# Kernel optimization log

Measured on AMD Instinct MI355X. Metric: run time of the kernel, lower is better.

Reference implementation:

```python
import jax, jax.numpy as jnp
import numpy as np

D_MODEL = 1024
NUM_HEADS = 16
D_K = D_MODEL // NUM_HEADS
D_FF = 4096
LN_EPS = 1e-5


def layer_norm(x, gamma, beta):
    mu = jnp.mean(x, axis=-1, keepdims=True)
    var = jnp.var(x, axis=-1, keepdims=True)
    return (x - mu) * jax.lax.rsqrt(var + LN_EPS) * gamma + beta


def setup_inputs() -> dict:
    key = jax.random.key(0)
    ks = jax.random.split(key, 10)
    s = 0.02
    return {
        "x": jax.random.normal(ks[0], (2, 2048, D_MODEL), dtype=jnp.float32),
        # per-head projections stacked: [H, d_model, d_k] (equivalent to the
        # num_heads separate nn.Linear(d_model, d_k, bias=False) modules)
        "Wq": jax.random.normal(ks[1], (NUM_HEADS, D_MODEL, D_K), dtype=jnp.float32) * s,
        "Wk": jax.random.normal(ks[2], (NUM_HEADS, D_MODEL, D_K), dtype=jnp.float32) * s,
        "Wv": jax.random.normal(ks[3], (NUM_HEADS, D_MODEL, D_K), dtype=jnp.float32) * s,
        "Wo": jax.random.normal(ks[4], (D_MODEL, D_MODEL), dtype=jnp.float32) * s,
        "W1": jax.random.normal(ks[5], (D_MODEL, D_FF), dtype=jnp.float32) * s,
        "b1": jnp.zeros((D_FF,), dtype=jnp.float32),
        "W2": jax.random.normal(ks[6], (D_FF, D_MODEL), dtype=jnp.float32) * s,
        "b2": jnp.zeros((D_MODEL,), dtype=jnp.float32),
        "g1": jnp.ones((D_MODEL,), dtype=jnp.float32),
        "beta1": jnp.zeros((D_MODEL,), dtype=jnp.float32),
        "g2": jnp.ones((D_MODEL,), dtype=jnp.float32),
        "beta2": jnp.zeros((D_MODEL,), dtype=jnp.float32),
    }


def reference(x, Wq, Wk, Wv, Wo, W1, b1, W2, b2, g1, beta1, g2, beta2):
    B, S, D = x.shape
    # ---- pre-LN multi-head self-attention ----
    h = layer_norm(x, g1, beta1)
    # batched QKV projections (equivalent to the per-head Python loop)
    Q = jnp.einsum('bsd,hdk->bhsk', h, Wq)  # [B,H,S,dk]
    K = jnp.einsum('bsd,hdk->bhsk', h, Wk)
    V = jnp.einsum('bsd,hdk->bhsk', h, Wv)
    scores = jnp.einsum('bhqk,bhsk->bhqs', Q, K) / jnp.sqrt(jnp.asarray(D_K, x.dtype))
    weights = jax.nn.softmax(scores, axis=-1)  # [B,H,S,S]
    attn = jnp.einsum('bhqs,bhsk->bhqk', weights, V)  # [B,H,S,dk]
    # concat heads along feature dim (head order preserved)
    concat = attn.transpose(0, 2, 1, 3).reshape(B, S, D)
    x = x + concat @ Wo
    # ---- pre-LN FFN (exact erf GELU, matching nn.GELU default) ----
    h2 = layer_norm(x, g2, beta2)
    ffn = jax.nn.gelu(h2 @ W1 + b1, approximate=False) @ W2 + b2
    return x + ffn
```

## Files before the change

### kernel.cpp

```cpp
#include <hip/hip_runtime.h>
#include <stdint.h>


typedef __attribute__((ext_vector_type(8))) short bf16x8;
typedef __attribute__((ext_vector_type(4))) float f32x4;
typedef __attribute__((ext_vector_type(16))) float f32x16;
typedef __attribute__((ext_vector_type(4))) unsigned short u16x4;
typedef __attribute__((ext_vector_type(4))) unsigned int u32x4;

#define DEV __device__ __forceinline__

static constexpr int DM   = 1024;
static constexpr int DFF  = 4096;
static constexpr int NH   = 16;
static constexpr int DKH  = 64;
static constexpr int SEQ  = 2048;
static constexpr int NBAT = 2;
static constexpr int NTOK = NBAT * SEQ;

DEV unsigned short f2bf(float f) {
  union { float f; unsigned int u; } v; v.f = f;
  unsigned int u = v.u;
  return (unsigned short)((u + 0x7fffu + ((u >> 16) & 1u)) >> 16);
}

DEV void gload_lds16(const unsigned short* g, unsigned short* l) {
  __builtin_amdgcn_global_load_lds(
      (const __attribute__((address_space(1))) unsigned int*)g,
      (__attribute__((address_space(3))) unsigned int*)l, 16, 0, 0);
}

DEV float fast_gelu(float x) {
  const float z = fabsf(x) * 0.70710678118654752f;
  const float t = __builtin_amdgcn_rcpf(1.0f + 0.3275911f * z);
  float p = 1.061405429f;
  p = p * t - 1.453152027f;
  p = p * t + 1.421413741f;
  p = p * t - 0.284496736f;
  p = p * t + 0.254829592f;
  p = p * t;
  float erfv = 1.0f - p * __expf(-z * z);
  erfv = copysignf(erfv, x);
  return 0.5f * x * (1.0f + erfv);
}

__global__ __launch_bounds__(256) void ln_kernel(
    const float* __restrict__ x, const float* __restrict__ g,
    const float* __restrict__ be, unsigned short* __restrict__ out) {
  const int row = blockIdx.x;
  const int t = threadIdx.x;
  const int lane = t & 63, w = t >> 6;
  const float4* xr = (const float4*)(x + (size_t)row * DM);
  float4 v = xr[t];
  float s  = v.x + v.y + v.z + v.w;
  float s2 = v.x * v.x + v.y * v.y + v.z * v.z + v.w * v.w;
#pragma unroll
  for (int off = 32; off; off >>= 1) {
    s  += __shfl_down(s, off);
    s2 += __shfl_down(s2, off);
  }
  __shared__ float rs_[4], rq_[4];
  if (lane == 0) { rs_[w] = s; rq_[w] = s2; }
  __syncthreads();
  float fs = rs_[0] + rs_[1] + rs_[2] + rs_[3];
  float fq = rq_[0] + rq_[1] + rq_[2] + rq_[3];
  float mu = fs * (1.0f / DM);
  float var = fq * (1.0f / DM) - mu * mu;
  float rstd = rsqrtf(var + 1e-5f);
  float4 gv = ((const float4*)g)[t];
  float4 bv = ((const float4*)be)[t];
  u16x4 o;
  o[0] = f2bf((v.x - mu) * rstd * gv.x + bv.x);
  o[1] = f2bf((v.y - mu) * rstd * gv.y + bv.y);
  o[2] = f2bf((v.z - mu) * rstd * gv.z + bv.z);
  o[3] = f2bf((v.w - mu) * rstd * gv.w + bv.w);
  *(u16x4*)(out + (size_t)row * DM + t * 4) = o;
}

__global__ __launch_bounds__(256) void transpose_weights(
    const float* __restrict__ Wq, const float* __restrict__ Wk,
    const float* __restrict__ Wv, const float* __restrict__ Wo,
    const float* __restrict__ W1, const float* __restrict__ W2,
    unsigned short* __restrict__ wqkv_t, unsigned short* __restrict__ wo_t,
    unsigned short* __restrict__ w1_t, unsigned short* __restrict__ w2_t) {
  __shared__ float lds[64][65];
  const int t = blockIdx.x;
  const float* inb; unsigned short* outb; int in_ld, out_ld;
  if (t < 768) {
    const int slice = t >> 4, tin = t & 15;
    const int which = slice >> 4, h = slice & 15;
    const float* W = (which == 0) ? Wq : (which == 1) ? Wk : Wv;
    inb = W + (size_t)((h << 10) + (tin << 6)) * 64;
    in_ld = 64;
    outb = wqkv_t + ((size_t)((which << 10) + (h << 6)) << 10) + (tin << 6);
    out_ld = 1024;
  } else if (t < 1024) {
    const int tt = t - 768, tr = tt >> 4, tc = tt & 15;
    inb = Wo + (size_t)(tc << 6) * 1024 + (tr << 6); in_ld = 1024;
    outb = wo_t + (size_t)(tr << 6) * 1024 + (tc << 6); out_ld = 1024;
  } else if (t < 2048) {
    const int tt = t - 1024, tr = tt >> 4, tc = tt & 15;
    inb = W1 + (size_t)(tc << 6) * 4096 + (tr << 6); in_ld = 4096;
    outb = w1_t + (size_t)(tr << 6) * 1024 + (tc << 6); out_ld = 1024;
  } else {
    const int tt = t - 2048, tr = tt >> 6, tc = tt & 63;
    inb = W2 + (size_t)(tc << 6) * 1024 + (tr << 6); in_ld = 1024;
    outb = w2_t + (size_t)(tr << 6) * 4096 + (tc << 6); out_ld = 4096;
  }
  const int j = threadIdx.x & 63, i0 = threadIdx.x >> 6;
#pragma unroll
  for (int p = 0; p < 16; ++p) {
    const int i = i0 + p * 4;
    lds[j][i] = inb[(size_t)i * in_ld + j];
  }
  __syncthreads();
#pragma unroll
  for (int p = 0; p < 16; ++p) {
    const int r = i0 + p * 4;
    outb[(size_t)r * out_ld + j] = f2bf(lds[r][j]);
  }
}

struct EpiArgs {
  unsigned short* q;
  unsigned short* k;
  unsigned short* vt;
  unsigned short* ob16;
  float* of32;
  float* p0;
  const float* bias;
  const float* resid;
};

template <int EPI>
DEV void epilogue_elem(float v, int row, int col, int N, int bz,
                       const EpiArgs& ep) {
  if constexpr (EPI == 0) {
    const int bb = row >> 11, rr = row & 2047;
    if (col < 1024) {
      const int hh = col >> 6, dk = col & 63;
      const int kk = dk >> 4, h8 = (dk >> 3) & 1, e = dk & 7;
      const int qblk = rr >> 5, l31 = rr & 31;
      ep.q[((size_t)(bb * NH + hh) * 64 + qblk) * 2048 + kk * 512 +
           (h8 * 32 + l31) * 8 + e] = f2bf(v * 0.18033688011112042f);
    } else if (col < 2048) {
      const int c = col - 1024;
      const int hh = c >> 6, dk = c & 63;
      const int kk = dk >> 4, h8 = (dk >> 3) & 1, e = dk & 7;
      const int kvblk = rr >> 5, l31 = rr & 31;
      ep.k[((size_t)(bb * NH + hh) * 64 + kvblk) * 2048 + kk * 512 +
           (h8 * 32 + l31) * 8 + e] = f2bf(v);
    } else {
      const int c = col - 2048, hh = c >> 6, dd = c & 63;
      const int ssw = (rr & ~12) | ((rr & 4) << 1) | ((rr & 8) >> 1);
      const int t64 = ssw >> 6, w = (ssw >> 4) & 3;
      const int h8 = (ssw >> 3) & 1, e = ssw & 7;
      const int dblk = dd >> 5, l31 = dd & 31;
      ep.vt[(((size_t)(bb * NH + hh) * 32 + t64) * 8 + dblk * 4 + w) * 512 +
            (h8 * 32 + l31) * 8 + e] = f2bf(v);
    }
  } else if constexpr (EPI == 1) {
    const size_t idx = (size_t)row * N + col;
    ep.of32[idx] = v + ep.resid[idx];
  } else if constexpr (EPI == 2) {
    ep.ob16[(size_t)row * N + col] = f2bf(fast_gelu(v + ep.bias[col]));
  } else {
    const size_t idx = (size_t)row * N + col;
    if (bz == 0) ep.p0[idx] = v;
    else ep.of32[idx] = ep.of32[idx] + v + ep.bias[col];
  }
}

template <int EPI>
__global__ __launch_bounds__(512, 2) void gemm_256(
    const unsigned short* __restrict__ A, const unsigned short* __restrict__ Bt,
    int N, int K, int ldk, EpiArgs ep) {
  __shared__ __align__(16) unsigned short Als[2][256 * 64];
  __shared__ __align__(16) unsigned short Bls[2][256 * 64];
  const int t = threadIdx.x, lane = t & 63, wave = t >> 6;
  const int wm = wave >> 2, wn = wave & 3;
  const int g = lane >> 4, r16 = lane & 15;
  const int nx = gridDim.x, nwg = nx * gridDim.y;
  int wgid = blockIdx.y * nx + blockIdx.x;
  wgid = (wgid & 7) * (nwg >> 3) + (wgid >> 3);
  const int m0 = (wgid / nx) * 256, n0 = (wgid % nx) * 256;

  f32x4 acc[8][4];
  const f32x4 z4 = {0.f, 0.f, 0.f, 0.f};
#pragma unroll
  for (int i = 0; i < 8; ++i)
#pragma unroll
    for (int j = 0; j < 4; ++j) acc[i][j] = z4;

  auto stage_half = [&](int b, int k0, int h) {
#pragma unroll
    for (int i = 0; i < 2; ++i) {
      const int c = i * 512 + t;
      const int row = c >> 3;
      const int sc = ((c & 7) ^ (row & 7)) * 8;
      const int dofs = ((h & 1) << 13) + (i * 512 + (wave << 6)) * 8;
      if (h < 2)
        gload_lds16(A + (size_t)(m0 + ((h & 1) << 7) + row) * ldk + k0 + sc,
                    &Als[b][dofs]);
      else
        gload_lds16(Bt + (size_t)(n0 + ((h & 1) << 7) + row) * ldk + k0 + sc,
                    &Bls[b][dofs]);
    }
  };

  const int NT = K >> 6;
#pragma unroll
  for (int h = 0; h < 4; ++h) stage_half(0, 0, h);

  for (int kt = 0; kt < NT; ++kt) {
    const int cur = kt & 1;
    const bool more = (kt + 1) < NT;
    const int nk0 = (kt + 1) << 6;
    __builtin_amdgcn_s_barrier();
    if (more) {
      stage_half(cur ^ 1, nk0, 0);
      stage_half(cur ^ 1, nk0, 1);
      asm volatile("s_waitcnt vmcnt(4)" ::: "memory");
    } else {
      asm volatile("s_waitcnt vmcnt(0)" ::: "memory");
    }
    __builtin_amdgcn_s_barrier();
    __builtin_amdgcn_sched_barrier(0);

    bf16x8 Af[8][2];
#pragma unroll
    for (int mf = 0; mf < 8; ++mf) {
      const int row = (wm << 7) + (mf << 4) + r16;
#pragma unroll
      for (int ks = 0; ks < 2; ++ks)
        Af[mf][ks] = *(const bf16x8*)
            &Als[cur][row * 64 + ((((ks << 2) | g) ^ (row & 7)) << 3)];
    }
#pragma unroll
    for (int qn = 0; qn < 2; ++qn) {
      bf16x8 Bf[2][2];
#pragma unroll
      for (int ni = 0; ni < 2; ++ni) {
        const int row = (wn << 6) + (((qn << 1) | ni) << 4) + r16;
#pragma unroll
        for (int ks = 0; ks < 2; ++ks)
          Bf[ni][ks] = *(const bf16x8*)
              &Bls[cur][row * 64 + ((((ks << 2) | g) ^ (row & 7)) << 3)];
      }
      __builtin_amdgcn_s_setprio(1);
#pragma unroll
      for (int ks = 0; ks < 2; ++ks)
#pragma unroll
        for (int mf = 0; mf < 8; ++mf)
#pragma unroll
          for (int ni = 0; ni < 2; ++ni)
            acc[mf][(qn << 1) | ni] = __builtin_amdgcn_mfma_f32_16x16x32_bf16(
                Af[mf][ks], Bf[ni][ks], acc[mf][(qn << 1) | ni], 0, 0, 0);
      __builtin_amdgcn_s_setprio(0);
      if (qn == 0 && more) {
        stage_half(cur ^ 1, nk0, 2);
        stage_half(cur ^ 1, nk0, 3);
      }
    }
  }
#pragma unroll
  for (int mf = 0; mf < 8; ++mf)
#pragma unroll
    for (int nf = 0; nf < 4; ++nf)
#pragma unroll
      for (int r = 0; r < 4; ++r)
        epilogue_elem<EPI>(acc[mf][nf][r],
                           m0 + (wm << 7) + (mf << 4) + (g << 2) + r,
                           n0 + (wn << 6) + (nf << 4) + r16, N, 0, ep);
}

template <int EPI>
__global__ __launch_bounds__(256) void gemm_pipe(
    const unsigned short* __restrict__ A, const unsigned short* __restrict__ Bt,
    int N, int Kc, int ldk, EpiArgs ep) {
  __shared__ __align__(16) unsigned short Als[2][128 * 64];
  __shared__ __align__(16) unsigned short Bls[2][128 * 64];
  const int t = threadIdx.x, lane = t & 63, wave = t >> 6;
  const int wm = wave >> 1, wn = wave & 1;
  const int g = lane >> 4, r16 = lane & 15;
  const int nx = gridDim.x;
  const int nwg = nx * gridDim.y;
  int wgid = blockIdx.y * nx + blockIdx.x;
  wgid = (wgid & 7) * (nwg >> 3) + (wgid >> 3);
  const int m0 = (wgid / nx) * 128, n0 = (wgid % nx) * 128;
  const int kbase = blockIdx.z * Kc;

  f32x4 acc[4][4];
  const f32x4 z4 = {0.f, 0.f, 0.f, 0.f};
#pragma unroll
  for (int i = 0; i < 4; ++i)
#pragma unroll
    for (int j = 0; j < 4; ++j) acc[i][j] = z4;

  auto stage = [&](int b, int k0) {
#pragma unroll
    for (int i = 0; i < 4; ++i) {
      const int cb = i * 256 + wave * 64;
      const int c = cb + lane;
      const int row = c >> 3;
      const int sc = ((c & 7) ^ (row & 7)) * 8;
      gload_lds16(A + (size_t)(m0 + row) * ldk + kbase + k0 + sc, &Als[b][cb * 8]);
      gload_lds16(Bt + (size_t)(n0 + row) * ldk + kbase + k0 + sc, &Bls[b][cb * 8]);
    }
  };

  const int NT = Kc >> 6;
  stage(0, 0);
  __syncthreads();
  for (int kt = 0; kt < NT; ++kt) {
    const int cur = kt & 1;
    if (kt + 1 < NT) stage(cur ^ 1, (kt + 1) << 6);
    const int sw = r16 & 7;
    bf16x8 af[2][4], bfr[2][4];
#pragma unroll
    for (int ks = 0; ks < 2; ++ks) {
#pragma unroll
      for (int mt = 0; mt < 4; ++mt)
        af[ks][mt] = *(const bf16x8*)&Als[cur][(wm * 64 + mt * 16 + r16) * 64 +
                                              (((ks << 2) | g) ^ sw) * 8];
#pragma unroll
      for (int nt = 0; nt < 4; ++nt)
        bfr[ks][nt] = *(const bf16x8*)&Bls[cur][(wn * 64 + nt * 16 + r16) * 64 +
                                               (((ks << 2) | g) ^ sw) * 8];
    }
    __builtin_amdgcn_s_setprio(1);
#pragma unroll
    for (int ks = 0; ks < 2; ++ks)
#pragma unroll
      for (int mt = 0; mt < 4; ++mt)
#pragma unroll
        for (int nt = 0; nt < 4; ++nt)
          acc[mt][nt] = __builtin_amdgcn_mfma_f32_16x16x32_bf16(
              af[ks][mt], bfr[ks][nt], acc[mt][nt], 0, 0, 0);
    __builtin_amdgcn_s_setprio(0);
    __syncthreads();
  }
#pragma unroll
  for (int mt = 0; mt < 4; ++mt)
#pragma unroll
    for (int nt = 0; nt < 4; ++nt)
#pragma unroll
      for (int r = 0; r < 4; ++r)
        epilogue_elem<EPI>(acc[mt][nt][r], m0 + wm * 64 + mt * 16 + g * 4 + r,
                           n0 + wn * 64 + nt * 16 + r16, N, blockIdx.z, ep);
}

__global__ __launch_bounds__(256) void reduce_add(const float* __restrict__ p,
                                                  float* __restrict__ out) {
  const int i = blockIdx.x * 256 + threadIdx.x;
  float4 a = ((const float4*)p)[i];
  float4 b = ((float4*)out)[i];
  b.x += a.x; b.y += a.y; b.z += a.z; b.w += a.w;
  ((float4*)out)[i] = b;
}

struct AttnState {
  f32x16 o0, o1;
  float m, lsum;
};

DEV void load_k(const unsigned short* kbase, int s, bf16x8 k0[4], bf16x8 k1[4]) {
  const unsigned short* p = kbase + (size_t)(s >> 5) * 2048;
#pragma unroll
  for (int kk = 0; kk < 4; ++kk) {
    k0[kk] = *(const bf16x8*)(p + kk * 512);
    k1[kk] = *(const bf16x8*)(p + 2048 + kk * 512);
  }
}

DEV void attn_tile(const bf16x8 k0[4], const bf16x8 k1[4],
                   const bf16x8 v0[4], const bf16x8 v1[4],
                   const bf16x8 qf[4], AttnState& st) {
  const f32x16 z16 = {0.f};
  f32x16 pA = z16, pB = z16;
  __builtin_amdgcn_s_setprio(1);
#pragma unroll
  for (int kk = 0; kk < 4; ++kk) {
    pA = __builtin_amdgcn_mfma_f32_32x32x16_bf16(k0[kk], qf[kk], pA, 0, 0, 0);
    pB = __builtin_amdgcn_mfma_f32_32x32x16_bf16(k1[kk], qf[kk], pB, 0, 0, 0);
  }
  __builtin_amdgcn_s_setprio(0);
  float m0 = fmaxf(pA[0], pB[0]), m1 = fmaxf(pA[1], pB[1]);
  float m2 = fmaxf(pA[2], pB[2]), m3 = fmaxf(pA[3], pB[3]);
#pragma unroll
  for (int r = 4; r < 16; r += 4) {
    m0 = fmaxf(m0, fmaxf(pA[r + 0], pB[r + 0]));
    m1 = fmaxf(m1, fmaxf(pA[r + 1], pB[r + 1]));
    m2 = fmaxf(m2, fmaxf(pA[r + 2], pB[r + 2]));
    m3 = fmaxf(m3, fmaxf(pA[r + 3], pB[r + 3]));
  }
  float mx = fmaxf(fmaxf(m0, m1), fmaxf(m2, m3));
  mx = fmaxf(mx, __shfl_xor(mx, 32));
  if (__any(mx > st.m + 11.5416f)) {
    const float mnew = fmaxf(st.m, mx);
    const float corr = exp2f(st.m - mnew);
#pragma unroll
    for (int r = 0; r < 16; ++r) { st.o0[r] *= corr; st.o1[r] *= corr; }
    st.lsum *= corr;
    st.m = mnew;
  }
  float ps = 0.f;
#pragma unroll
  for (int r = 0; r < 16; ++r) {
    pA[r] = exp2f(pA[r] - st.m); ps += pA[r];
    pB[r] = exp2f(pB[r] - st.m); ps += pB[r];
  }
  ps += __shfl_xor(ps, 32);
  st.lsum += ps;
  bf16x8 pw[4];
#pragma unroll
  for (int w = 0; w < 4; ++w) {
    unsigned int wd0, wd1, wd2, wd3;
    const int e0 = (w & 1) * 8;
    if (w < 2) {
      asm("v_cvt_pk_bf16_f32 %0, %1, %2" : "=v"(wd0) : "v"(pA[e0 + 0]), "v"(pA[e0 + 1]));
      asm("v_cvt_pk_bf16_f32 %0, %1, %2" : "=v"(wd1) : "v"(pA[e0 + 2]), "v"(pA[e0 + 3]));
      asm("v_cvt_pk_bf16_f32 %0, %1, %2" : "=v"(wd2) : "v"(pA[e0 + 4]), "v"(pA[e0 + 5]));
      asm("v_cvt_pk_bf16_f32 %0, %1, %2" : "=v"(wd3) : "v"(pA[e0 + 6]), "v"(pA[e0 + 7]));
    } else {
      asm("v_cvt_pk_bf16_f32 %0, %1, %2" : "=v"(wd0) : "v"(pB[e0 + 0]), "v"(pB[e0 + 1]));
      asm("v_cvt_pk_bf16_f32 %0, %1, %2" : "=v"(wd1) : "v"(pB[e0 + 2]), "v"(pB[e0 + 3]));
      asm("v_cvt_pk_bf16_f32 %0, %1, %2" : "=v"(wd2) : "v"(pB[e0 + 4]), "v"(pB[e0 + 5]));
      asm("v_cvt_pk_bf16_f32 %0, %1, %2" : "=v"(wd3) : "v"(pB[e0 + 6]), "v"(pB[e0 + 7]));
    }
    u32x4 wv = {wd0, wd1, wd2, wd3};
    pw[w] = __builtin_bit_cast(bf16x8, wv);
  }
  __builtin_amdgcn_s_setprio(1);
#pragma unroll
  for (int w = 0; w < 4; ++w) {
    st.o0 = __builtin_amdgcn_mfma_f32_32x32x16_bf16(v0[w], pw[w], st.o0, 0, 0, 0);
    st.o1 = __builtin_amdgcn_mfma_f32_32x32x16_bf16(v1[w], pw[w], st.o1, 0, 0, 0);
  }
  __builtin_amdgcn_s_setprio(0);
}

__global__ __launch_bounds__(256, 2) void attn_kernel(
    const unsigned short* __restrict__ Qc, const unsigned short* __restrict__ Kc,
    const unsigned short* __restrict__ Vt, unsigned short* __restrict__ Oc) {
  const int lane = threadIdx.x & 63, wave = threadIdx.x >> 6;
  const int hi = lane >> 5, l31 = lane & 31;
  const int i = blockIdx.x;
  const int k8 = i & 7, mq = i >> 3;
  const int grp = k8 + 8 * (mq >> 4);
  const int qb = mq & 15;
  const int b = grp >> 4, h = grp & 15;
  const int q0 = qb * 128 + wave * 32;

  const unsigned short* qbp = Qc + ((size_t)grp * 64 + (q0 >> 5)) * 2048 + lane * 8;
  const unsigned short* kbp = Kc + (size_t)grp * 64 * 2048 + lane * 8;
  const unsigned short* vbp = Vt + (size_t)grp * 32 * 4096 + lane * 8;

  bf16x8 qf[4];
#pragma unroll
  for (int kk = 0; kk < 4; ++kk) qf[kk] = *(const bf16x8*)(qbp + kk * 512);

  AttnState st;
#pragma unroll
  for (int r = 0; r < 16; ++r) { st.o0[r] = 0.f; st.o1[r] = 0.f; }
  st.m = -1e30f; st.lsum = 0.f;

  bf16x8 kA0[4], kA1[4], kB0[4], kB1[4];
  load_k(kbp, 0, kA0, kA1);

  for (int s0 = 0; s0 < SEQ; s0 += 128) {
    const unsigned short* vt0 = vbp + (size_t)(s0 >> 6) * 4096;
    bf16x8 v0[4], v1[4];
#pragma unroll
    for (int w = 0; w < 4; ++w) {
      v0[w] = *(const bf16x8*)(vt0 + w * 512);
      v1[w] = *(const bf16x8*)(vt0 + 2048 + w * 512);
    }
    load_k(kbp, s0 + 64, kB0, kB1);
    attn_tile(kA0, kA1, v0, v1, qf, st);
    const unsigned short* vt1 = vbp + (size_t)((s0 + 64) >> 6) * 4096;
#pragma unroll
    for (int w = 0; w < 4; ++w) {
      v0[w] = *(const bf16x8*)(vt1 + w * 512);
      v1[w] = *(const bf16x8*)(vt1 + 2048 + w * 512);
    }
    const int snext = (s0 + 128 < SEQ) ? (s0 + 128) : 0;
    load_k(kbp, snext, kA0, kA1);
    attn_tile(kB0, kB1, v0, v1, qf, st);
  }

  const float inv = 1.0f / st.lsum;
  const size_t rowbase = (size_t)b * SEQ;
  unsigned short* op = Oc + (rowbase + q0 + l31) * DM + h * DKH + hi * 4;
#pragma unroll
  for (int dblk = 0; dblk < 2; ++dblk)
#pragma unroll
    for (int g4 = 0; g4 < 4; ++g4) {
      u16x4 stv;
#pragma unroll
      for (int r = 0; r < 4; ++r) {
        const float v = (dblk ? st.o1[g4 * 4 + r] : st.o0[g4 * 4 + r]) * inv;
        stv[r] = f2bf(v);
      }
      *(u16x4*)(op + dblk * 32 + g4 * 8) = stv;
    }
}

extern "C" void kernel_launch(void* const* d_in, const int* in_sizes, int n_in,
                              void* d_out, int out_size, void* d_ws,
                              size_t ws_size, hipStream_t stream) {
  (void)in_sizes; (void)n_in; (void)out_size; (void)ws_size;
  const float* x   = (const float*)d_in[0];
  const float* Wq  = (const float*)d_in[1];
  const float* Wk  = (const float*)d_in[2];
  const float* Wv  = (const float*)d_in[3];
  const float* Wo  = (const float*)d_in[4];
  const float* W1  = (const float*)d_in[5];
  const float* b1  = (const float*)d_in[6];
  const float* W2  = (const float*)d_in[7];
  const float* b2  = (const float*)d_in[8];
  const float* g1  = (const float*)d_in[9];
  const float* be1 = (const float*)d_in[10];
  const float* g2  = (const float*)d_in[11];
  const float* be2 = (const float*)d_in[12];
  float* out = (float*)d_out;

  char* ws = (char*)d_ws;
  const size_t MB = 1024 * 1024;
  unsigned short* h_buf  = (unsigned short*)(ws + 0 * MB);
  unsigned short* wqkv_t = (unsigned short*)(ws + 8 * MB);
  unsigned short* wo_t   = (unsigned short*)(ws + 14 * MB);
  unsigned short* w1_t   = (unsigned short*)(ws + 16 * MB);
  unsigned short* w2_t   = (unsigned short*)(ws + 24 * MB);
  unsigned short* q_attn = (unsigned short*)(ws + 32 * MB);
  unsigned short* k_attn = (unsigned short*)(ws + 40 * MB);
  unsigned short* v_attn = (unsigned short*)(ws + 48 * MB);
  unsigned short* ffn1   = (unsigned short*)(ws + 32 * MB);
  float*          p0     = (float*)(ws + 0 * MB);

  EpiArgs e0 = {}; e0.q = q_attn; e0.k = k_attn; e0.vt = v_attn;
  EpiArgs e1 = {}; e1.of32 = out; e1.resid = x;
  EpiArgs e2 = {}; e2.ob16 = ffn1; e2.bias = b1;
  EpiArgs e4 = {}; e4.of32 = out; e4.p0 = p0; e4.bias = b2;

  transpose_weights<<<3072, 256, 0, stream>>>(Wq, Wk, Wv, Wo, W1, W2,
                                              wqkv_t, wo_t, w1_t, w2_t);
  ln_kernel<<<NTOK, 256, 0, stream>>>(x, g1, be1, h_buf);
  gemm_256<0><<<dim3(3072 / 256, NTOK / 256), 512, 0, stream>>>(
      h_buf, wqkv_t, 3072, DM, DM, e0);
  attn_kernel<<<512, 256, 0, stream>>>(q_attn, k_attn, v_attn, h_buf);
  gemm_pipe<1><<<dim3(DM / 128, NTOK / 128, 1), 256, 0, stream>>>(
      h_buf, wo_t, DM, DM, DM, e1);
  ln_kernel<<<NTOK, 256, 0, stream>>>(out, g2, be2, h_buf);
  gemm_256<2><<<dim3(DFF / 256, NTOK / 256), 512, 0, stream>>>(
      h_buf, w1_t, DFF, DM, DM, e2);
  gemm_pipe<4><<<dim3(DM / 128, NTOK / 128, 2), 256, 0, stream>>>(
      ffn1, w2_t, DM, DFF / 2, DFF, e4);
  reduce_add<<<4096, 256, 0, stream>>>(p0, out);
}
```

Before: 264.7 us.

## Split attention KV range across two wave halves and merge softmax states in LDS

The attention kernel now launches 512 threads per block. The two halves of the waves each process half of the key/value sequence for the same query rows, and their partial max, sum and output accumulators are merged through shared memory before the store. This doubles the waves available per CU for the 512-block grid, which is meant to hide latency in the attention phase. It adds an LDS round-trip, a block barrier and a merge step. The exp2f calls are also replaced with the hardware exp2 builtin.

```diff
diff --git a/kernel.cpp b/kernel.cpp
--- a/kernel.cpp
+++ b/kernel.cpp
@@ -398,7 +398,7 @@
   mx = fmaxf(mx, __shfl_xor(mx, 32));
   if (__any(mx > st.m + 11.5416f)) {
     const float mnew = fmaxf(st.m, mx);
-    const float corr = exp2f(st.m - mnew);
+    const float corr = __builtin_amdgcn_exp2f(st.m - mnew);
 #pragma unroll
     for (int r = 0; r < 16; ++r) { st.o0[r] *= corr; st.o1[r] *= corr; }
     st.lsum *= corr;
@@ -407,8 +407,8 @@
   float ps = 0.f;
 #pragma unroll
   for (int r = 0; r < 16; ++r) {
-    pA[r] = exp2f(pA[r] - st.m); ps += pA[r];
-    pB[r] = exp2f(pB[r] - st.m); ps += pB[r];
+    pA[r] = __builtin_amdgcn_exp2f(pA[r] - st.m); ps += pA[r];
+    pB[r] = __builtin_amdgcn_exp2f(pB[r] - st.m); ps += pB[r];
   }
   ps += __shfl_xor(ps, 32);
   st.lsum += ps;
@@ -440,17 +440,19 @@
   __builtin_amdgcn_s_setprio(0);
 }
 
-__global__ __launch_bounds__(256, 2) void attn_kernel(
+__global__ __launch_bounds__(512, 4) void attn_kernel(
     const unsigned short* __restrict__ Qc, const unsigned short* __restrict__ Kc,
     const unsigned short* __restrict__ Vt, unsigned short* __restrict__ Oc) {
-  const int lane = threadIdx.x & 63, wave = threadIdx.x >> 6;
+  const int t = threadIdx.x;
+  const int lane = t & 63, wave = t >> 6;
+  const int qw = wave & 3, half = wave >> 2;
   const int hi = lane >> 5, l31 = lane & 31;
   const int i = blockIdx.x;
   const int k8 = i & 7, mq = i >> 3;
   const int grp = k8 + 8 * (mq >> 4);
   const int qb = mq & 15;
   const int b = grp >> 4, h = grp & 15;
-  const int q0 = qb * 128 + wave * 32;
+  const int q0 = qb * 128 + qw * 32;
 
   const unsigned short* qbp = Qc + ((size_t)grp * 64 + (q0 >> 5)) * 2048 + lane * 8;
   const unsigned short* kbp = Kc + (size_t)grp * 64 * 2048 + lane * 8;
@@ -465,10 +467,11 @@
   for (int r = 0; r < 16; ++r) { st.o0[r] = 0.f; st.o1[r] = 0.f; }
   st.m = -1e30f; st.lsum = 0.f;
 
+  const int sbase = half << 10;
   bf16x8 kA0[4], kA1[4], kB0[4], kB1[4];
-  load_k(kbp, 0, kA0, kA1);
-
-  for (int s0 = 0; s0 < SEQ; s0 += 128) {
+  load_k(kbp, sbase, kA0, kA1);
+
+  for (int s0 = sbase; s0 < sbase + 1024; s0 += 128) {
     const unsigned short* vt0 = vbp + (size_t)(s0 >> 6) * 4096;
     bf16x8 v0[4], v1[4];
 #pragma unroll
@@ -484,26 +487,46 @@
       v0[w] = *(const bf16x8*)(vt1 + w * 512);
       v1[w] = *(const bf16x8*)(vt1 + 2048 + w * 512);
     }
-    const int snext = (s0 + 128 < SEQ) ? (s0 + 128) : 0;
+    const int snext = (s0 + 128 < sbase + 1024) ? (s0 + 128) : sbase;
     load_k(kbp, snext, kA0, kA1);
     attn_tile(kB0, kB1, v0, v1, qf, st);
   }
 
-  const float inv = 1.0f / st.lsum;
-  const size_t rowbase = (size_t)b * SEQ;
-  unsigned short* op = Oc + (rowbase + q0 + l31) * DM + h * DKH + hi * 4;
-#pragma unroll
-  for (int dblk = 0; dblk < 2; ++dblk)
-#pragma unroll
-    for (int g4 = 0; g4 < 4; ++g4) {
-      u16x4 stv;
-#pragma unroll
-      for (int r = 0; r < 4; ++r) {
-        const float v = (dblk ? st.o1[g4 * 4 + r] : st.o0[g4 * 4 + r]) * inv;
-        stv[r] = f2bf(v);
+  __shared__ float mls[4][2][64];
+  __shared__ float obuf[4][64][33];
+  if (half == 1) {
+    mls[qw][0][lane] = st.m;
+    mls[qw][1][lane] = st.lsum;
+#pragma unroll
+    for (int r = 0; r < 16; ++r) {
+      obuf[qw][lane][r] = st.o0[r];
+      obuf[qw][lane][16 + r] = st.o1[r];
+    }
+  }
+  __syncthreads();
+  if (half == 0) {
+    const float mb = mls[qw][0][lane], lb = mls[qw][1][lane];
+    const float mm = fmaxf(st.m, mb);
+    const float ca = __builtin_amdgcn_exp2f(st.m - mm);
+    const float cb = __builtin_amdgcn_exp2f(mb - mm);
+    const float inv = 1.0f / (st.lsum * ca + lb * cb);
+    const size_t rowbase = (size_t)b * SEQ;
+    unsigned short* op = Oc + (rowbase + q0 + l31) * DM + h * DKH + hi * 4;
+#pragma unroll
+    for (int dblk = 0; dblk < 2; ++dblk)
+#pragma unroll
+      for (int g4 = 0; g4 < 4; ++g4) {
+        u16x4 stv;
+#pragma unroll
+        for (int r = 0; r < 4; ++r) {
+          const int e = g4 * 4 + r;
+          const float va = dblk ? st.o1[e] : st.o0[e];
+          const float vb = obuf[qw][lane][dblk * 16 + e];
+          stv[r] = f2bf((va * ca + vb * cb) * inv);
+        }
+        *(u16x4*)(op + dblk * 32 + g4 * 8) = stv;
       }
-      *(u16x4*)(op + dblk * 32 + g4 * 8) = stv;
-    }
+  }
 }
 
 extern "C" void kernel_launch(void* const* d_in, const int* in_sizes, int n_in,
@@ -548,7 +571,7 @@
   ln_kernel<<<NTOK, 256, 0, stream>>>(x, g1, be1, h_buf);
   gemm_256<0><<<dim3(3072 / 256, NTOK / 256), 512, 0, stream>>>(
       h_buf, wqkv_t, 3072, DM, DM, e0);
-  attn_kernel<<<512, 256, 0, stream>>>(q_attn, k_attn, v_attn, h_buf);
+  attn_kernel<<<512, 512, 0, stream>>>(q_attn, k_attn, v_attn, h_buf);
   gemm_pipe<1><<<dim3(DM / 128, NTOK / 128, 1), 256, 0, stream>>>(
       h_buf, wo_t, DM, DM, DM, e1);
   ln_kernel<<<NTOK, 256, 0, stream>>>(out, g2, be2, h_buf);
```

Measured after the change: 427.3 us. +61.4%, slower.
